# Performance work log

Measured on AMD Instinct MI355X. Metric: run time of the kernel, lower is better.

The kernel has to match this reference:

```python
import jax, jax.numpy as jnp
import numpy as np

B, S, E, H = 2, 2048, 1024, 16
D = E // H  # head_dim = 64


def setup_inputs() -> dict:
    key = jax.random.key(0)
    ks = jax.random.split(key, 5)
    return {
        "hidden_states": jax.random.normal(ks[0], (B, S, E), jnp.float32),
        "c_attn_w": jax.random.normal(ks[1], (E, 3 * E), jnp.float32) * 0.02,
        "c_attn_b": jnp.zeros((3 * E,), jnp.float32),
        "c_proj_w": jax.random.normal(ks[2], (E, E), jnp.float32) * 0.02,
        "c_proj_b": jnp.zeros((E,), jnp.float32),
    }


def reference(hidden_states, c_attn_w, c_attn_b, c_proj_w, c_proj_b):
    # Conv1D: x @ w + b -> qkv [B, S, 3E]
    qkv = hidden_states @ c_attn_w + c_attn_b
    q, k, v = jnp.split(qkv, 3, axis=-1)
    # [B, H, S, D]
    q = q.reshape(B, S, H, D).transpose(0, 2, 1, 3)
    k = k.reshape(B, S, H, D).transpose(0, 2, 1, 3)
    v = v.reshape(B, S, H, D).transpose(0, 2, 1, 3)
    # scores [B, H, S, S], scaled by sqrt(head_dim)
    scores = jnp.einsum("bhqd,bhkd->bhqk", q, k) / jnp.sqrt(jnp.asarray(D, q.dtype))
    causal = jnp.tril(jnp.ones((S, S), bool))  # [S, S]
    mask_value = jnp.finfo(scores.dtype).min
    scores = jnp.where(causal, scores, mask_value)
    attn = jax.nn.softmax(scores, axis=-1)
    # attn @ V -> [B, H, S, D] -> [B, S, E]
    out = jnp.einsum("bhqk,bhkd->bhqd", attn, v)
    out = out.transpose(0, 2, 1, 3).reshape(B, S, E)
    return out @ c_proj_w + c_proj_b
```

## Files before the change

kernel.cpp:

```cpp
#include <hip/hip_runtime.h>

using bf16 = __bf16;
typedef __bf16 bf16x8 __attribute__((ext_vector_type(8)));
typedef __bf16 bf16x4 __attribute__((ext_vector_type(4)));
typedef float  f32x4  __attribute__((ext_vector_type(4)));

#define MFMA16(a, b, c) __builtin_amdgcn_mfma_f32_16x16x32_bf16((a), (b), (c), 0, 0, 0)

static constexpr int S = 2048, E = 1024;
static constexpr float CSCALE = 0.18033688011112042f;

__device__ __forceinline__ void gld16(const bf16* g, bf16* l) {
    __builtin_amdgcn_global_load_lds((const __attribute__((address_space(1))) unsigned*)g,
                                     (__attribute__((address_space(3))) unsigned*)l, 16, 0, 0);
}

__global__ __launch_bounds__(256) void k_prep(const float* __restrict__ hs, const float* __restrict__ w0,
                                              const float* __restrict__ w1, bf16* __restrict__ A0,
                                              bf16* __restrict__ Wt0, bf16* __restrict__ Wt1) {
    __shared__ float tile[64][33];
    const int bx = blockIdx.x;
    if (bx < 4096) {
        int i = (bx * 256 + threadIdx.x) * 4;
        float4 v = *(const float4*)(hs + i);
        bf16x4 o = { (bf16)v.x, (bf16)v.y, (bf16)v.z, (bf16)v.w };
        *(bf16x4*)(A0 + i) = o;
        return;
    }
    const float* in;
    bf16* outp;
    int K, N, nb, kb;
    const int j = bx - 4096;
    if (j < 1536) { in = w0; outp = Wt0; K = 1024; N = 3072; nb = j % 96; kb = j / 96; }
    else          { in = w1; outp = Wt1; K = 1024; N = 1024; nb = (j - 1536) % 32; kb = (j - 1536) / 32; }
    const int bxx = nb * 32, byy = kb * 64;
    {
        const int r0 = threadIdx.x >> 5, c = threadIdx.x & 31;
#pragma unroll
        for (int i = 0; i < 8; i++)
            tile[r0 + i * 8][c] = in[(long)(byy + r0 + i * 8) * N + bxx + c];
    }
    __syncthreads();
    {
        const int n0 = threadIdx.x >> 6, k = threadIdx.x & 63;
#pragma unroll
        for (int i = 0; i < 8; i++) {
            const int n = n0 + i * 4;
            outp[(long)(bxx + n) * K + byy + k] = (bf16)tile[k][n];
        }
    }
}

__global__ __launch_bounds__(256) void k_gemm_qkv(const bf16* __restrict__ A, const bf16* __restrict__ Bt,
                                                  const float* __restrict__ bias, bf16* __restrict__ Qs,
                                                  bf16* __restrict__ Kf, bf16* __restrict__ Vf, int Kk) {
    const int bm = blockIdx.x * 128;
    const int bn = blockIdx.y * 128;
    const int tid = threadIdx.x;
    const int w = tid >> 6, lane = tid & 63;
    const int wm = (w >> 1) * 64, wn = (w & 1) * 64;
    const int col = lane & 15, quad = lane >> 4;

    __shared__ __align__(16) char smem[32768];
    bf16* sA = (bf16*)smem;
    bf16* sB = (bf16*)(smem + 16384);
    bf16* T  = (bf16*)smem;

    const bf16* pA[4]; const bf16* pB[4]; bf16* lA[4]; bf16* lB[4];
#pragma unroll
    for (int i = 0; i < 4; i++) {
        const int c = i * 256 + w * 64 + lane;
        const int r = c >> 3, sl = (c & 7) ^ (r & 7);
        pA[i] = A  + (long)(bm + r) * Kk + sl * 8;
        pB[i] = Bt + (long)(bn + r) * Kk + sl * 8;
        lA[i] = sA + i * 2048 + w * 512;
        lB[i] = sB + i * 2048 + w * 512;
    }

    f32x4 acc[4][4] = {};

    for (int k0 = 0; k0 < Kk; k0 += 64) {
        __syncthreads();
#pragma unroll
        for (int i = 0; i < 4; i++) gld16(pA[i] + k0, lA[i]);
#pragma unroll
        for (int i = 0; i < 4; i++) gld16(pB[i] + k0, lB[i]);
        __syncthreads();
#pragma unroll
        for (int h = 0; h < 2; h++) {
            bf16x8 af[4], bfr[4];
#pragma unroll
            for (int mt = 0; mt < 4; mt++) {
                const int row = wm + mt * 16 + col;
                af[mt] = *(const bf16x8*)(sA + row * 64 + (((h * 4 + quad) ^ (col & 7)) * 8));
            }
#pragma unroll
            for (int nt = 0; nt < 4; nt++) {
                const int row = wn + nt * 16 + col;
                bfr[nt] = *(const bf16x8*)(sB + row * 64 + (((h * 4 + quad) ^ (col & 7)) * 8));
            }
#pragma unroll
            for (int mt = 0; mt < 4; mt++)
#pragma unroll
                for (int nt = 0; nt < 4; nt++)
                    acc[mt][nt] = MFMA16(af[mt], bfr[nt], acc[mt][nt]);
        }
    }

    const int seg = bn >> 10;
    const int b = bm >> 11;
    const int kt0 = (bm & 2047) >> 6;

    if (seg == 0) {
#pragma unroll
        for (int mt = 0; mt < 4; mt++) {
            const int gr = bm + wm + mt * 16 + quad * 4;
#pragma unroll
            for (int nt = 0; nt < 4; nt++) {
                const int gc = bn + wn + nt * 16 + col;
                const float bv = bias[gc];
#pragma unroll
                for (int r = 0; r < 4; r++)
                    Qs[(long)(gr + r) * 1024 + gc] = (bf16)((acc[mt][nt][r] + bv) * CSCALE);
            }
        }
        return;
    }

    const int hl = w >> 1;
    if (seg == 1) {
        const int bh = b * 16 + (bn >> 6) - 16 + hl;
#pragma unroll 1
        for (int p = 0; p < 2; p++) {
            __syncthreads();
            if ((wm >> 6) == p) {
#pragma unroll
                for (int mt = 0; mt < 4; mt++) {
                    const int sl = mt * 16 + quad * 4;
#pragma unroll
                    for (int nt = 0; nt < 4; nt++) {
                        const int gcl = wn + nt * 16 + col;
                        const float bv = bias[bn + gcl];
#pragma unroll
                        for (int r = 0; r < 4; r++)
                            T[(sl + r) * 136 + gcl] = (bf16)(acc[mt][nt][r] + bv);
                    }
                }
            }
            __syncthreads();
            const int ktp = kt0 + p;
#pragma unroll
            for (int mi = 0; mi < 2; mi++) {
                const int mt = (w & 1) * 2 + mi;
#pragma unroll
                for (int half = 0; half < 2; half++) {
                    bf16x8 ch = *(const bf16x8*)(T + (mt * 16 + col) * 136 + hl * 64 + half * 32 + quad * 8);
                    const long chunk = ((long)(bh * 32 + ktp) * 8 + mt * 2 + half) * 64 + lane;
                    *(bf16x8*)(Kf + chunk * 8) = ch;
                }
            }
        }
    } else {
        const int bh = b * 16 + (bn >> 6) - 32 + hl;
#pragma unroll 1
        for (int p = 0; p < 2; p++) {
            __syncthreads();
            if ((wm >> 6) == p) {
#pragma unroll
                for (int mt = 0; mt < 4; mt++) {
                    const int sl = mt * 16 + quad * 4;
#pragma unroll
                    for (int nt = 0; nt < 4; nt++) {
                        const int gcl = wn + nt * 16 + col;
                        const float bv = bias[bn + gcl];
                        bf16x4 pk = { (bf16)(acc[mt][nt][0] + bv), (bf16)(acc[mt][nt][1] + bv),
                                      (bf16)(acc[mt][nt][2] + bv), (bf16)(acc[mt][nt][3] + bv) };
                        *(bf16x4*)(T + gcl * 72 + sl) = pk;
                    }
                }
            }
            __syncthreads();
            const int ktp = kt0 + p;
#pragma unroll
            for (int di = 0; di < 2; di++) {
                const int dt = (w & 1) * 2 + di;
#pragma unroll
                for (int ks = 0; ks < 2; ks++) {
                    bf16x8 ch = *(const bf16x8*)(T + (hl * 64 + dt * 16 + col) * 72 + ks * 32 + quad * 8);
                    const long chunk = ((long)(bh * 32 + ktp) * 8 + dt * 2 + ks) * 64 + lane;
                    *(bf16x8*)(Vf + chunk * 8) = ch;
                }
            }
        }
    }
}

__global__ __launch_bounds__(256) void k_gemm_bt64(const bf16* __restrict__ A, const bf16* __restrict__ Bt,
                                                    const float* __restrict__ bias, float* __restrict__ Cout,
                                                    int Mm, int Nn, int Kk) {
    const int bm = blockIdx.x * 64;
    const int bn = blockIdx.y * 128;
    const int tid = threadIdx.x;
    const int w = tid >> 6, lane = tid & 63;
    const int wm = (w >> 1) * 32, wn = (w & 1) * 64;
    const int col = lane & 15, quad = lane >> 4;

    __shared__ bf16 sA[64 * 64];
    __shared__ bf16 sB[128 * 64];

    const bf16* pA[2]; bf16* lA[2];
#pragma unroll
    for (int i = 0; i < 2; i++) {
        const int c = i * 256 + w * 64 + lane;
        const int r = c >> 3, sl = (c & 7) ^ (r & 7);
        pA[i] = A + (long)(bm + r) * Kk + sl * 8;
        lA[i] = sA + i * 2048 + w * 512;
    }
    const bf16* pB[4]; bf16* lB[4];
#pragma unroll
    for (int i = 0; i < 4; i++) {
        const int c = i * 256 + w * 64 + lane;
        const int r = c >> 3, sl = (c & 7) ^ (r & 7);
        pB[i] = Bt + (long)(bn + r) * Kk + sl * 8;
        lB[i] = sB + i * 2048 + w * 512;
    }

    f32x4 acc[2][4] = {};

    for (int k0 = 0; k0 < Kk; k0 += 64) {
        __syncthreads();
#pragma unroll
        for (int i = 0; i < 2; i++) gld16(pA[i] + k0, lA[i]);
#pragma unroll
        for (int i = 0; i < 4; i++) gld16(pB[i] + k0, lB[i]);
        __syncthreads();
#pragma unroll
        for (int h = 0; h < 2; h++) {
            bf16x8 af[2], bfr[4];
#pragma unroll
            for (int mt = 0; mt < 2; mt++) {
                const int row = wm + mt * 16 + col;
                af[mt] = *(const bf16x8*)(sA + row * 64 + (((h * 4 + quad) ^ (col & 7)) * 8));
            }
#pragma unroll
            for (int nt = 0; nt < 4; nt++) {
                const int row = wn + nt * 16 + col;
                bfr[nt] = *(const bf16x8*)(sB + row * 64 + (((h * 4 + quad) ^ (col & 7)) * 8));
            }
#pragma unroll
            for (int mt = 0; mt < 2; mt++)
#pragma unroll
                for (int nt = 0; nt < 4; nt++)
                    acc[mt][nt] = MFMA16(af[mt], bfr[nt], acc[mt][nt]);
        }
    }

#pragma unroll
    for (int mt = 0; mt < 2; mt++) {
        const int gr = bm + wm + mt * 16 + quad * 4;
#pragma unroll
        for (int nt = 0; nt < 4; nt++) {
            const int gc = bn + wn + nt * 16 + col;
            const float bv = bias[gc];
#pragma unroll
            for (int r = 0; r < 4; r++)
                Cout[(long)(gr + r) * Nn + gc] = acc[mt][nt][r] + bv;
        }
    }
}

__global__ __launch_bounds__(128) void k_attn(const bf16* __restrict__ Qs, const bf16* __restrict__ Kf,
                                              const bf16* __restrict__ Vf, bf16* __restrict__ out) {
    const int bh = blockIdx.x & 31;
    const int t = 63 - (blockIdx.x >> 5);
    const int b = bh >> 4, h = bh & 15;
    const int tid = threadIdx.x;
    const int w = tid >> 6, lane = tid & 63;
    const int col = lane & 15, quad = lane >> 4;
    const int q0 = t * 32;
    const int nkt = (t >> 1) + 1;
    const int kA = nkt >> 1;
    const int kbeg = w ? kA : 0;
    const int kend = w ? nkt : kA;

    __shared__ bf16 sP[2][32 * 72];
    __shared__ float M[64][36];
    bf16* pw = sP[w];

    const bf16* kfb = Kf + ((long)bh << 17) + lane * 8;
    const bf16* vfb = Vf + ((long)bh << 17) + lane * 8;

    bf16x8 bq[2][2];
#pragma unroll
    for (int qg = 0; qg < 2; qg++) {
        const bf16* qp = Qs + (long)(b * S + q0 + qg * 16 + col) * E + h * 64 + quad * 8;
        bq[qg][0] = *(const bf16x8*)(qp);
        bq[qg][1] = *(const bf16x8*)(qp + 32);
    }
    float m_[2] = { -1e30f, -1e30f }, l_[2] = { 0.f, 0.f };
    f32x4 o[2][4] = {};

#pragma unroll 1
    for (int kt = kbeg; kt < kend; kt++) {
        bf16x8 kfr[4][2], vfr[4][2];
#pragma unroll
        for (int mt = 0; mt < 4; mt++)
#pragma unroll
            for (int half = 0; half < 2; half++)
                kfr[mt][half] = *(const bf16x8*)(kfb + ((long)(kt * 8 + mt * 2 + half) << 9));
#pragma unroll
        for (int dt = 0; dt < 4; dt++)
#pragma unroll
            for (int ks = 0; ks < 2; ks++)
                vfr[dt][ks] = *(const bf16x8*)(vfb + ((long)(kt * 8 + dt * 2 + ks) << 9));

        f32x4 s[2][4];
#pragma unroll
        for (int mt = 0; mt < 4; mt++)
#pragma unroll
            for (int qg = 0; qg < 2; qg++) {
                f32x4 z = {};
                z = MFMA16(kfr[mt][0], bq[qg][0], z);
                z = MFMA16(kfr[mt][1], bq[qg][1], z);
                s[qg][mt] = z;
            }
        if (kt == nkt - 1) {
#pragma unroll
            for (int qg = 0; qg < 2; qg++) {
                const int qrow = q0 + qg * 16 + col;
#pragma unroll
                for (int mt = 0; mt < 4; mt++)
#pragma unroll
                    for (int r = 0; r < 4; r++)
                        if (kt * 64 + mt * 16 + quad * 4 + r > qrow) s[qg][mt][r] = -1e30f;
            }
        }
#pragma unroll
        for (int qg = 0; qg < 2; qg++) {
            float cm = -1e30f;
#pragma unroll
            for (int mt = 0; mt < 4; mt++)
#pragma unroll
                for (int r = 0; r < 4; r++) cm = fmaxf(cm, s[qg][mt][r]);
            cm = fmaxf(cm, __shfl_xor(cm, 16));
            cm = fmaxf(cm, __shfl_xor(cm, 32));
            const float mnew = fmaxf(m_[qg], cm);
            const float alpha = __builtin_amdgcn_exp2f(m_[qg] - mnew);
            m_[qg] = mnew;
            float rs = 0.f;
#pragma unroll
            for (int mt = 0; mt < 4; mt++)
#pragma unroll
                for (int r = 0; r < 4; r++) {
                    float pe = __builtin_amdgcn_exp2f(s[qg][mt][r] - mnew);
                    s[qg][mt][r] = pe;
                    rs += pe;
                }
            l_[qg] = l_[qg] * alpha + rs;
#pragma unroll
            for (int dt = 0; dt < 4; dt++)
#pragma unroll
                for (int r = 0; r < 4; r++) o[qg][dt][r] *= alpha;
#pragma unroll
            for (int mt = 0; mt < 4; mt++) {
                bf16x4 pk = { (bf16)s[qg][mt][0], (bf16)s[qg][mt][1],
                              (bf16)s[qg][mt][2], (bf16)s[qg][mt][3] };
                *(bf16x4*)(pw + (qg * 16 + col) * 72 + mt * 16 + quad * 4) = pk;
            }
        }
#pragma unroll
        for (int ks = 0; ks < 2; ks++) {
            bf16x8 ap[2];
#pragma unroll
            for (int qg = 0; qg < 2; qg++)
                ap[qg] = *(const bf16x8*)(pw + (qg * 16 + col) * 72 + ks * 32 + quad * 8);
#pragma unroll
            for (int dt = 0; dt < 4; dt++)
#pragma unroll
                for (int qg = 0; qg < 2; qg++)
                    o[qg][dt] = MFMA16(vfr[dt][ks], ap[qg], o[qg][dt]);
        }
    }

#pragma unroll
    for (int qg = 0; qg < 2; qg++) {
        float lt = l_[qg];
        lt += __shfl_xor(lt, 16);
        lt += __shfl_xor(lt, 32);
        l_[qg] = lt;
    }

    if (w == 0) {
#pragma unroll
        for (int qg = 0; qg < 2; qg++) {
#pragma unroll
            for (int dt = 0; dt < 4; dt++)
                *(f32x4*)&M[lane][qg * 16 + dt * 4] = o[qg][dt];
            M[lane][32 + qg * 2] = m_[qg];
            M[lane][33 + qg * 2] = l_[qg];
        }
    }
    __syncthreads();
    if (w == 1) {
#pragma unroll
        for (int qg = 0; qg < 2; qg++) {
            const float m0 = M[lane][32 + qg * 2];
            const float l0 = M[lane][33 + qg * 2];
            const float mm = fmaxf(m0, m_[qg]);
            const float a0 = __builtin_amdgcn_exp2f(m0 - mm);
            const float a1 = __builtin_amdgcn_exp2f(m_[qg] - mm);
            const float li = 1.f / (l0 * a0 + l_[qg] * a1);
            bf16* op = out + (long)(b * S + q0 + qg * 16 + col) * E + h * 64 + quad * 4;
#pragma unroll
            for (int dt = 0; dt < 4; dt++) {
                f32x4 o0 = *(const f32x4*)&M[lane][qg * 16 + dt * 4];
                bf16x4 ov;
#pragma unroll
                for (int r = 0; r < 4; r++)
                    ov[r] = (bf16)((o0[r] * a0 + o[qg][dt][r] * a1) * li);
                *(bf16x4*)(op + dt * 16) = ov;
            }
        }
    }
}

extern "C" void kernel_launch(void* const* d_in, const int* in_sizes, int n_in,
                              void* d_out, int out_size, void* d_ws, size_t ws_size,
                              hipStream_t stream) {
    const float* hs = (const float*)d_in[0];
    const float* w0 = (const float*)d_in[1];
    const float* b0 = (const float*)d_in[2];
    const float* w1 = (const float*)d_in[3];
    const float* b1 = (const float*)d_in[4];
    float* outp = (float*)d_out;

    char* ws = (char*)d_ws;
    bf16* A0    = (bf16*)(ws);
    bf16* Wt0   = (bf16*)(ws + 8388608);
    bf16* Wt1   = (bf16*)(ws + 14680064);
    bf16* Qs    = (bf16*)(ws + 16777216);
    bf16* Kf    = (bf16*)(ws + 25165824);
    bf16* Vf    = (bf16*)(ws + 33554432);
    bf16* attnO = (bf16*)(ws + 41943040);

    k_prep<<<6144, 256, 0, stream>>>(hs, w0, w1, A0, Wt0, Wt1);
    k_gemm_qkv<<<dim3(32, 24), 256, 0, stream>>>(A0, Wt0, b0, Qs, Kf, Vf, 1024);
    k_attn<<<2048, 128, 0, stream>>>(Qs, Kf, Vf, attnO);
    k_gemm_bt64<<<dim3(64, 8), 256, 0, stream>>>(attnO, Wt1, b1, outp, 4096, 1024, 1024);
}
```

Measured before the change: 180.2 us.

## Share double-buffered LDS K/V tiles across two query-block waves in attention

```diff
diff --git a/kernel.cpp b/kernel.cpp
--- a/kernel.cpp
+++ b/kernel.cpp
@@ -272,19 +272,17 @@
 __global__ __launch_bounds__(128) void k_attn(const bf16* __restrict__ Qs, const bf16* __restrict__ Kf,
                                               const bf16* __restrict__ Vf, bf16* __restrict__ out) {
     const int bh = blockIdx.x & 31;
-    const int t = 63 - (blockIdx.x >> 5);
+    const int t = 31 - (blockIdx.x >> 5);
     const int b = bh >> 4, h = bh & 15;
     const int tid = threadIdx.x;
     const int w = tid >> 6, lane = tid & 63;
     const int col = lane & 15, quad = lane >> 4;
-    const int q0 = t * 32;
-    const int nkt = (t >> 1) + 1;
-    const int kA = nkt >> 1;
-    const int kbeg = w ? kA : 0;
-    const int kend = w ? nkt : kA;
-
-    __shared__ bf16 sP[2][32 * 72];
-    __shared__ float M[64][36];
+    const int q0 = t * 64 + w * 32;
+    const int nkt = t + 1;
+
+    __shared__ bf16 sK[2][4096];
+    __shared__ bf16 sV[2][4096];
+    __shared__ bf16 sP[2][2048];
     bf16* pw = sP[w];
 
     const bf16* kfb = Kf + ((long)bh << 17) + lane * 8;
@@ -300,19 +298,37 @@
     float m_[2] = { -1e30f, -1e30f }, l_[2] = { 0.f, 0.f };
     f32x4 o[2][4] = {};
 
+#pragma unroll
+    for (int j = 0; j < 4; j++) {
+        const int c = j * 2 + w;
+        gld16(kfb + (long)c * 512, sK[0] + c * 512);
+        gld16(vfb + (long)c * 512, sV[0] + c * 512);
+    }
+
 #pragma unroll 1
-    for (int kt = kbeg; kt < kend; kt++) {
+    for (int kt = 0; kt < nkt; kt++) {
+        const int buf = kt & 1;
+        __syncthreads();
+        if (kt + 1 < nkt) {
+#pragma unroll
+            for (int j = 0; j < 4; j++) {
+                const int c = j * 2 + w;
+                gld16(kfb + ((long)(kt + 1) * 8 + c) * 512, sK[buf ^ 1] + c * 512);
+                gld16(vfb + ((long)(kt + 1) * 8 + c) * 512, sV[buf ^ 1] + c * 512);
+            }
+        }
+
         bf16x8 kfr[4][2], vfr[4][2];
 #pragma unroll
         for (int mt = 0; mt < 4; mt++)
 #pragma unroll
             for (int half = 0; half < 2; half++)
-                kfr[mt][half] = *(const bf16x8*)(kfb + ((long)(kt * 8 + mt * 2 + half) << 9));
+                kfr[mt][half] = *(const bf16x8*)(sK[buf] + (mt * 2 + half) * 512 + lane * 8);
 #pragma unroll
         for (int dt = 0; dt < 4; dt++)
 #pragma unroll
             for (int ks = 0; ks < 2; ks++)
-                vfr[dt][ks] = *(const bf16x8*)(vfb + ((long)(kt * 8 + dt * 2 + ks) << 9));
+                vfr[dt][ks] = *(const bf16x8*)(sV[buf] + (dt * 2 + ks) * 512 + lane * 8);
 
         f32x4 s[2][4];
 #pragma unroll
@@ -363,17 +379,21 @@
                 for (int r = 0; r < 4; r++) o[qg][dt][r] *= alpha;
 #pragma unroll
             for (int mt = 0; mt < 4; mt++) {
+                const int q = qg * 16 + col;
+                const int cl = mt * 2 + (quad >> 1);
                 bf16x4 pk = { (bf16)s[qg][mt][0], (bf16)s[qg][mt][1],
                               (bf16)s[qg][mt][2], (bf16)s[qg][mt][3] };
-                *(bf16x4*)(pw + (qg * 16 + col) * 72 + mt * 16 + quad * 4) = pk;
+                *(bf16x4*)(pw + q * 64 + ((cl ^ (q & 7)) * 8 + (quad & 1) * 4)) = pk;
             }
         }
 #pragma unroll
         for (int ks = 0; ks < 2; ks++) {
             bf16x8 ap[2];
 #pragma unroll
-            for (int qg = 0; qg < 2; qg++)
-                ap[qg] = *(const bf16x8*)(pw + (qg * 16 + col) * 72 + ks * 32 + quad * 8);
+            for (int qg = 0; qg < 2; qg++) {
+                const int q = qg * 16 + col;
+                ap[qg] = *(const bf16x8*)(pw + q * 64 + (((ks * 4 + quad) ^ (q & 7)) * 8));
+            }
 #pragma unroll
             for (int dt = 0; dt < 4; dt++)
 #pragma unroll
@@ -387,39 +407,13 @@
         float lt = l_[qg];
         lt += __shfl_xor(lt, 16);
         lt += __shfl_xor(lt, 32);
-        l_[qg] = lt;
-    }
-
-    if (w == 0) {
-#pragma unroll
-        for (int qg = 0; qg < 2; qg++) {
-#pragma unroll
-            for (int dt = 0; dt < 4; dt++)
-                *(f32x4*)&M[lane][qg * 16 + dt * 4] = o[qg][dt];
-            M[lane][32 + qg * 2] = m_[qg];
-            M[lane][33 + qg * 2] = l_[qg];
-        }
-    }
-    __syncthreads();
-    if (w == 1) {
-#pragma unroll
-        for (int qg = 0; qg < 2; qg++) {
-            const float m0 = M[lane][32 + qg * 2];
-            const float l0 = M[lane][33 + qg * 2];
-            const float mm = fmaxf(m0, m_[qg]);
-            const float a0 = __builtin_amdgcn_exp2f(m0 - mm);
-            const float a1 = __builtin_amdgcn_exp2f(m_[qg] - mm);
-            const float li = 1.f / (l0 * a0 + l_[qg] * a1);
-            bf16* op = out + (long)(b * S + q0 + qg * 16 + col) * E + h * 64 + quad * 4;
-#pragma unroll
-            for (int dt = 0; dt < 4; dt++) {
-                f32x4 o0 = *(const f32x4*)&M[lane][qg * 16 + dt * 4];
-                bf16x4 ov;
-#pragma unroll
-                for (int r = 0; r < 4; r++)
-                    ov[r] = (bf16)((o0[r] * a0 + o[qg][dt][r] * a1) * li);
-                *(bf16x4*)(op + dt * 16) = ov;
-            }
+        const float li = 1.f / lt;
+        bf16* op = out + (long)(b * S + q0 + qg * 16 + col) * E + h * 64 + quad * 4;
+#pragma unroll
+        for (int dt = 0; dt < 4; dt++) {
+            bf16x4 ov = { (bf16)(o[qg][dt][0] * li), (bf16)(o[qg][dt][1] * li),
+                          (bf16)(o[qg][dt][2] * li), (bf16)(o[qg][dt][3] * li) };
+            *(bf16x4*)(op + dt * 16) = ov;
         }
     }
 }
@@ -445,6 +439,6 @@
 
     k_prep<<<6144, 256, 0, stream>>>(hs, w0, w1, A0, Wt0, Wt1);
     k_gemm_qkv<<<dim3(32, 24), 256, 0, stream>>>(A0, Wt0, b0, Qs, Kf, Vf, 1024);
-    k_attn<<<2048, 128, 0, stream>>>(Qs, Kf, Vf, attnO);
+    k_attn<<<1024, 128, 0, stream>>>(Qs, Kf, Vf, attnO);
     k_gemm_bt64<<<dim3(64, 8), 256, 0, stream>>>(attnO, Wt1, b1, outp, 4096, 1024, 1024);
 }
```

Result: slower. 193.1 us (+7.2%).

## Double attention query tile to 64 rows and swizzle P tile in LDS

Applied to the files above, without the earlier changes.

```diff
diff --git a/kernel.cpp b/kernel.cpp
--- a/kernel.cpp
+++ b/kernel.cpp
@@ -269,36 +269,36 @@
     }
 }
 
-__global__ __launch_bounds__(128) void k_attn(const bf16* __restrict__ Qs, const bf16* __restrict__ Kf,
-                                              const bf16* __restrict__ Vf, bf16* __restrict__ out) {
+__global__ __launch_bounds__(128, 2) void k_attn(const bf16* __restrict__ Qs, const bf16* __restrict__ Kf,
+                                                 const bf16* __restrict__ Vf, bf16* __restrict__ out) {
     const int bh = blockIdx.x & 31;
-    const int t = 63 - (blockIdx.x >> 5);
+    const int t = blockIdx.x >> 5;
     const int b = bh >> 4, h = bh & 15;
     const int tid = threadIdx.x;
     const int w = tid >> 6, lane = tid & 63;
     const int col = lane & 15, quad = lane >> 4;
-    const int q0 = t * 32;
-    const int nkt = (t >> 1) + 1;
+    const int q0 = t * 64;
+    const int nkt = t + 1;
     const int kA = nkt >> 1;
     const int kbeg = w ? kA : 0;
     const int kend = w ? nkt : kA;
 
-    __shared__ bf16 sP[2][32 * 72];
-    __shared__ float M[64][36];
+    __shared__ bf16 sP[2][4096];
+    __shared__ float M[64][73];
     bf16* pw = sP[w];
 
     const bf16* kfb = Kf + ((long)bh << 17) + lane * 8;
     const bf16* vfb = Vf + ((long)bh << 17) + lane * 8;
 
-    bf16x8 bq[2][2];
-#pragma unroll
-    for (int qg = 0; qg < 2; qg++) {
+    bf16x8 bq[4][2];
+#pragma unroll
+    for (int qg = 0; qg < 4; qg++) {
         const bf16* qp = Qs + (long)(b * S + q0 + qg * 16 + col) * E + h * 64 + quad * 8;
         bq[qg][0] = *(const bf16x8*)(qp);
         bq[qg][1] = *(const bf16x8*)(qp + 32);
     }
-    float m_[2] = { -1e30f, -1e30f }, l_[2] = { 0.f, 0.f };
-    f32x4 o[2][4] = {};
+    float m_[4] = { -1e30f, -1e30f, -1e30f, -1e30f }, l_[4] = { 0.f, 0.f, 0.f, 0.f };
+    f32x4 o[4][4] = {};
 
 #pragma unroll 1
     for (int kt = kbeg; kt < kend; kt++) {
@@ -314,34 +314,29 @@
             for (int ks = 0; ks < 2; ks++)
                 vfr[dt][ks] = *(const bf16x8*)(vfb + ((long)(kt * 8 + dt * 2 + ks) << 9));
 
-        f32x4 s[2][4];
-#pragma unroll
-        for (int mt = 0; mt < 4; mt++)
-#pragma unroll
-            for (int qg = 0; qg < 2; qg++) {
+#pragma unroll
+        for (int qg = 0; qg < 4; qg++) {
+            f32x4 s[4];
+#pragma unroll
+            for (int mt = 0; mt < 4; mt++) {
                 f32x4 z = {};
                 z = MFMA16(kfr[mt][0], bq[qg][0], z);
                 z = MFMA16(kfr[mt][1], bq[qg][1], z);
-                s[qg][mt] = z;
-            }
-        if (kt == nkt - 1) {
-#pragma unroll
-            for (int qg = 0; qg < 2; qg++) {
+                s[mt] = z;
+            }
+            if (kt == nkt - 1) {
                 const int qrow = q0 + qg * 16 + col;
 #pragma unroll
                 for (int mt = 0; mt < 4; mt++)
 #pragma unroll
                     for (int r = 0; r < 4; r++)
-                        if (kt * 64 + mt * 16 + quad * 4 + r > qrow) s[qg][mt][r] = -1e30f;
-            }
-        }
-#pragma unroll
-        for (int qg = 0; qg < 2; qg++) {
+                        if (kt * 64 + mt * 16 + quad * 4 + r > qrow) s[mt][r] = -1e30f;
+            }
             float cm = -1e30f;
 #pragma unroll
             for (int mt = 0; mt < 4; mt++)
 #pragma unroll
-                for (int r = 0; r < 4; r++) cm = fmaxf(cm, s[qg][mt][r]);
+                for (int r = 0; r < 4; r++) cm = fmaxf(cm, s[mt][r]);
             cm = fmaxf(cm, __shfl_xor(cm, 16));
             cm = fmaxf(cm, __shfl_xor(cm, 32));
             const float mnew = fmaxf(m_[qg], cm);
@@ -352,8 +347,8 @@
             for (int mt = 0; mt < 4; mt++)
 #pragma unroll
                 for (int r = 0; r < 4; r++) {
-                    float pe = __builtin_amdgcn_exp2f(s[qg][mt][r] - mnew);
-                    s[qg][mt][r] = pe;
+                    float pe = __builtin_amdgcn_exp2f(s[mt][r] - mnew);
+                    s[mt][r] = pe;
                     rs += pe;
                 }
             l_[qg] = l_[qg] * alpha + rs;
@@ -361,29 +356,29 @@
             for (int dt = 0; dt < 4; dt++)
 #pragma unroll
                 for (int r = 0; r < 4; r++) o[qg][dt][r] *= alpha;
+            const int q = qg * 16 + col;
 #pragma unroll
             for (int mt = 0; mt < 4; mt++) {
-                bf16x4 pk = { (bf16)s[qg][mt][0], (bf16)s[qg][mt][1],
-                              (bf16)s[qg][mt][2], (bf16)s[qg][mt][3] };
-                *(bf16x4*)(pw + (qg * 16 + col) * 72 + mt * 16 + quad * 4) = pk;
+                const int cl = mt * 2 + (quad >> 1);
+                bf16x4 pk = { (bf16)s[mt][0], (bf16)s[mt][1], (bf16)s[mt][2], (bf16)s[mt][3] };
+                *(bf16x4*)(pw + q * 64 + ((cl ^ (q & 7)) * 8 + (quad & 1) * 4)) = pk;
             }
         }
 #pragma unroll
         for (int ks = 0; ks < 2; ks++) {
-            bf16x8 ap[2];
-#pragma unroll
-            for (int qg = 0; qg < 2; qg++)
-                ap[qg] = *(const bf16x8*)(pw + (qg * 16 + col) * 72 + ks * 32 + quad * 8);
-#pragma unroll
-            for (int dt = 0; dt < 4; dt++)
-#pragma unroll
-                for (int qg = 0; qg < 2; qg++)
-                    o[qg][dt] = MFMA16(vfr[dt][ks], ap[qg], o[qg][dt]);
-        }
-    }
-
-#pragma unroll
-    for (int qg = 0; qg < 2; qg++) {
+#pragma unroll
+            for (int qg = 0; qg < 4; qg++) {
+                const int q = qg * 16 + col;
+                const bf16x8 ap = *(const bf16x8*)(pw + q * 64 + (((ks * 4 + quad) ^ (q & 7)) * 8));
+#pragma unroll
+                for (int dt = 0; dt < 4; dt++)
+                    o[qg][dt] = MFMA16(vfr[dt][ks], ap, o[qg][dt]);
+            }
+        }
+    }
+
+#pragma unroll
+    for (int qg = 0; qg < 4; qg++) {
         float lt = l_[qg];
         lt += __shfl_xor(lt, 16);
         lt += __shfl_xor(lt, 32);
@@ -392,20 +387,22 @@
 
     if (w == 0) {
 #pragma unroll
-        for (int qg = 0; qg < 2; qg++) {
+        for (int qg = 0; qg < 4; qg++) {
 #pragma unroll
             for (int dt = 0; dt < 4; dt++)
-                *(f32x4*)&M[lane][qg * 16 + dt * 4] = o[qg][dt];
-            M[lane][32 + qg * 2] = m_[qg];
-            M[lane][33 + qg * 2] = l_[qg];
+#pragma unroll
+                for (int r = 0; r < 4; r++)
+                    M[lane][(qg * 4 + dt) * 4 + r] = o[qg][dt][r];
+            M[lane][64 + qg * 2] = m_[qg];
+            M[lane][65 + qg * 2] = l_[qg];
         }
     }
     __syncthreads();
     if (w == 1) {
 #pragma unroll
-        for (int qg = 0; qg < 2; qg++) {
-            const float m0 = M[lane][32 + qg * 2];
-            const float l0 = M[lane][33 + qg * 2];
+        for (int qg = 0; qg < 4; qg++) {
+            const float m0 = M[lane][64 + qg * 2];
+            const float l0 = M[lane][65 + qg * 2];
             const float mm = fmaxf(m0, m_[qg]);
             const float a0 = __builtin_amdgcn_exp2f(m0 - mm);
             const float a1 = __builtin_amdgcn_exp2f(m_[qg] - mm);
@@ -413,11 +410,10 @@
             bf16* op = out + (long)(b * S + q0 + qg * 16 + col) * E + h * 64 + quad * 4;
 #pragma unroll
             for (int dt = 0; dt < 4; dt++) {
-                f32x4 o0 = *(const f32x4*)&M[lane][qg * 16 + dt * 4];
                 bf16x4 ov;
 #pragma unroll
                 for (int r = 0; r < 4; r++)
-                    ov[r] = (bf16)((o0[r] * a0 + o[qg][dt][r] * a1) * li);
+                    ov[r] = (bf16)((M[lane][(qg * 4 + dt) * 4 + r] * a0 + o[qg][dt][r] * a1) * li);
                 *(bf16x4*)(op + dt * 16) = ov;
             }
         }
@@ -445,6 +441,6 @@
 
     k_prep<<<6144, 256, 0, stream>>>(hs, w0, w1, A0, Wt0, Wt1);
     k_gemm_qkv<<<dim3(32, 24), 256, 0, stream>>>(A0, Wt0, b0, Qs, Kf, Vf, 1024);
-    k_attn<<<2048, 128, 0, stream>>>(Qs, Kf, Vf, attnO);
+    k_attn<<<1024, 128, 0, stream>>>(Qs, Kf, Vf, attnO);
     k_gemm_bt64<<<dim3(64, 8), 256, 0, stream>>>(attnO, Wt1, b1, outp, 4096, 1024, 1024);
 }
```

Result: slower. 186.4 us (+3.4%).
